# Performance work log

Measured on AMD Instinct MI355X. Metric: run time of the kernel, lower is better.

The kernel has to match this reference:

```python
import jax, jax.numpy as jnp
import numpy as np

B, C, H, W = 4, 512, 128, 128
CI = C // 2   # inter_planes
CQ = C // 8   # q/k dim in CrossAttention


def conv1x1(x, w, b=None):
    # x: [B,Cin,H,W], w: [Cout,Cin]
    y = jnp.einsum('oc,bchw->bohw', w, x)
    if b is not None:
        y = y + b[None, :, None, None]
    return y


def setup_inputs() -> dict:
    key = jax.random.key(0)
    ks = jax.random.split(key, 13)
    s = 0.05
    return {
        'x': jax.random.normal(ks[0], (B, C, H, W), jnp.float32),
        # SCCA gating params (1x1 convs, no bias except conv_up)
        'w_q_right': jax.random.normal(ks[1], (1, C), jnp.float32) * s,
        'w_v_right': jax.random.normal(ks[2], (CI, C), jnp.float32) * s,
        'w_up': jax.random.normal(ks[3], (C, CI), jnp.float32) * s,
        'b_up': jnp.zeros((C,), jnp.float32),
        'w_q_left': jax.random.normal(ks[4], (CI, C), jnp.float32) * s,
        'w_v_left': jax.random.normal(ks[5], (CI, C), jnp.float32) * s,
        # CrossAttention params (1x1 convs with bias)
        'wq': jax.random.normal(ks[6], (CQ, C), jnp.float32) * s,
        'bq': jnp.zeros((CQ,), jnp.float32),
        'wk': jax.random.normal(ks[7], (CQ, C), jnp.float32) * s,
        'bk': jnp.zeros((CQ,), jnp.float32),
        'wv': jax.random.normal(ks[8], (C, C), jnp.float32) * s,
        'bv': jnp.zeros((C,), jnp.float32),
        'gamma': jnp.asarray(0.5, jnp.float32),
    }


def cross_attention(x, wq, bq, wk, bk, wv, bv, gamma):
    # criss-cross attention: each pixel attends to its row and column
    b, c, h, w = x.shape
    q = conv1x1(x, wq, bq)   # [B,CQ,H,W]
    k = conv1x1(x, wk, bk)   # [B,CQ,H,W]
    v = conv1x1(x, wv, bv)   # [B,C,H,W]
    # column (H) affinities with -inf on the self diagonal (as in INF())
    diag = jnp.where(jnp.eye(h, dtype=bool), -jnp.inf, 0.0).astype(x.dtype)
    e_h = jnp.einsum('bchw,bcgw->bhwg', q, k) + diag[None, :, None, :]  # [B,H,W,H]
    e_w = jnp.einsum('bchw,bchv->bhwv', q, k)                            # [B,H,W,W]
    att = jax.nn.softmax(jnp.concatenate([e_h, e_w], axis=-1), axis=-1)  # [B,H,W,H+W]
    a_h, a_w = att[..., :h], att[..., h:]
    out_h = jnp.einsum('bcgw,bhwg->bchw', v, a_h)
    out_w = jnp.einsum('bchv,bhwv->bchw', v, a_w)
    return gamma * (out_h + out_w) + x


def spatial_weighted(x, w_q_right, w_v_right, w_up, b_up):
    b, c, h, w = x.shape
    input_x = conv1x1(x, w_v_right).reshape(b, CI, h * w)       # [B,CI,HW]
    mask = jax.nn.softmax(conv1x1(x, w_q_right).reshape(b, h * w), axis=-1)  # [B,HW]
    ctx = jnp.einsum('bcn,bn->bc', input_x, mask)               # [B,CI]
    ctx = jnp.einsum('oc,bc->bo', w_up, ctx) + b_up             # [B,C]
    mask_ch = jax.nn.sigmoid(ctx)[:, :, None, None]
    return x * mask_ch


def channel_weighted(x, w_q_left, w_v_left):
    b, c, h, w = x.shape
    g_x = conv1x1(x, w_q_left)                                  # [B,CI,H,W]
    avg = g_x.mean(axis=(2, 3))                                 # [B,CI]
    theta = conv1x1(x, w_v_left).reshape(b, CI, h * w)          # [B,CI,HW]
    ctx = jax.nn.softmax(jnp.einsum('bc,bcn->bn', avg, theta), axis=-1)
    mask_sp = jax.nn.sigmoid(ctx).reshape(b, 1, h, w)
    return x * mask_sp


def reference(x, w_q_right, w_v_right, w_up, b_up, w_q_left, w_v_left,
              wq, bq, wk, bk, wv, bv, gamma):
    cc = spatial_weighted(x, w_q_right, w_v_right, w_up, b_up)
    cc = cross_attention(cc, wq, bq, wk, bk, wv, bv, gamma)
    cs = channel_weighted(x, w_q_left, w_v_left)
    cs = cross_attention(cs, wq, bq, wk, bk, wv, bv, gamma)
    out = cs + cc
    out = cross_attention(out, wq, bq, wk, bk, wv, bv, gamma)
    return out
```

## Files before the change

kernel.cpp:

```cpp
#include <hip/hip_runtime.h>
#include <hip/hip_bf16.h>
#include <math.h>

typedef __hip_bfloat16 bf16;
typedef __attribute__((ext_vector_type(8))) short s16x8;
typedef __attribute__((ext_vector_type(4))) float f32x4;

constexpr int Bn  = 4;
constexpr int Cn  = 512;
constexpr int Hn  = 128;
constexpr int Wn  = 128;
constexpr int Nn  = Hn * Wn;
constexpr int CQn = 64;
constexpr int CIn = 256;

__device__ __forceinline__ float bf2f(bf16 v){ return __bfloat162float(v); }
__device__ __forceinline__ bf16  f2bf(float v){ return __float2bfloat16(v); }

__device__ __forceinline__ void gload_lds16(const void* g, void* l){
  __builtin_amdgcn_global_load_lds(
      (const __attribute__((address_space(1))) unsigned int*)g,
      (__attribute__((address_space(3))) unsigned int*)l,
      16, 0, 0);
}


__global__ __launch_bounds__(256) void k_dotc2(const float* __restrict__ x,
                                               const float* __restrict__ w,
                                               int wstride,
                                               float* __restrict__ part){
  int t = blockIdx.x * 256 + threadIdx.x;
  int half = blockIdx.y;
  int b = t >> 14;
  const float* wp = w + (size_t)b * wstride + half * 256;
  const float* xp = x + (size_t)b * Cn * Nn + (size_t)(half * 256) * Nn + (t & (Nn - 1));
  float acc = 0.f;
  #pragma unroll 16
  for (int c = 0; c < 256; ++c) acc += wp[c] * xp[(size_t)c * Nn];
  part[(size_t)half * (Bn * Nn) + t] = acc;
}

__global__ __launch_bounds__(256) void k_dotcadd(const float* __restrict__ part,
                                                 float* __restrict__ out){
  int t = blockIdx.x * 256 + threadIdx.x;
  out[t] = part[t] + part[(size_t)Bn * Nn + t];
}

__global__ __launch_bounds__(256) void k_rowmean(const float* __restrict__ x,
                                                 float* __restrict__ out,
                                                 float scale){
  int bc = blockIdx.x;
  const float* xp = x + (size_t)bc * Nn;
  float acc = 0.f;
  for (int n = threadIdx.x; n < Nn; n += 256) acc += xp[n];
  for (int o = 32; o > 0; o >>= 1) acc += __shfl_down(acc, o);
  __shared__ float red[4];
  if ((threadIdx.x & 63) == 0) red[threadIdx.x >> 6] = acc;
  __syncthreads();
  if (threadIdx.x == 0) out[bc] = (red[0] + red[1] + red[2] + red[3]) * scale;
}

__global__ __launch_bounds__(256) void k_rowdot(const float* __restrict__ W,
                                                const float* __restrict__ vec,
                                                float* __restrict__ out){
  __shared__ float vs[Cn];
  int b = blockIdx.x, t = threadIdx.x;
  for (int j = t; j < Cn; j += 256) vs[j] = vec[b * Cn + j];
  __syncthreads();
  const float4* wp = (const float4*)(W + (size_t)t * Cn);
  float a = 0.f;
  #pragma unroll 4
  for (int j = 0; j < Cn / 4; ++j){
    float4 w4 = wp[j];
    a += w4.x * vs[4*j] + w4.y * vs[4*j+1] + w4.z * vs[4*j+2] + w4.w * vs[4*j+3];
  }
  out[b * CIn + t] = a;
}

__global__ __launch_bounds__(256) void k_coldot(const float* __restrict__ W,
                                                const float* __restrict__ vec,
                                                float* __restrict__ out){
  __shared__ float vs[CIn];
  int b = blockIdx.y, t = threadIdx.x;
  int c = blockIdx.x * 256 + t;
  if (t < CIn) vs[t] = vec[b * CIn + t];
  __syncthreads();
  float a = 0.f;
  #pragma unroll 8
  for (int j = 0; j < CIn; ++j) a += W[(size_t)j * Cn + c] * vs[j];
  out[b * Cn + c] = a;
}

__global__ __launch_bounds__(256) void k_mch2(const float* __restrict__ w_up,
                                              const float* __restrict__ b_up,
                                              const float* __restrict__ ctx,
                                              float* __restrict__ mch){
  __shared__ float cs[CIn];
  int b = blockIdx.y, t = threadIdx.x;
  int o = blockIdx.x * 256 + t;
  if (t < CIn) cs[t] = ctx[b * CIn + t];
  __syncthreads();
  const float4* wp = (const float4*)(w_up + (size_t)o * CIn);
  float a = b_up[o];
  #pragma unroll 4
  for (int j = 0; j < CIn / 4; ++j){
    float4 w4 = wp[j];
    a += w4.x * cs[4*j] + w4.y * cs[4*j+1] + w4.z * cs[4*j+2] + w4.w * cs[4*j+3];
  }
  mch[b * Cn + o] = 1.f / (1.f + expf(-a));
}

__global__ __launch_bounds__(1024) void k_stats(const float* __restrict__ vv,
                                                float* __restrict__ stats){
  int b = blockIdx.x;
  const float* pp = vv + (size_t)b * Nn;
  int t = threadIdx.x;
  float m = -3.4e38f;
  for (int n = t; n < Nn; n += 1024) m = fmaxf(m, pp[n]);
  for (int o = 32; o > 0; o >>= 1) m = fmaxf(m, __shfl_down(m, o));
  __shared__ float red[16];
  int wid = t >> 6, lid = t & 63;
  if (lid == 0) red[wid] = m;
  __syncthreads();
  if (t == 0){
    float q = red[0];
    for (int i = 1; i < 16; i++) q = fmaxf(q, red[i]);
    red[0] = q;
  }
  __syncthreads();
  m = red[0];
  __syncthreads();
  float s = 0.f;
  for (int n = t; n < Nn; n += 1024) s += expf(pp[n] - m);
  for (int o = 32; o > 0; o >>= 1) s += __shfl_down(s, o);
  if (lid == 0) red[wid] = s;
  __syncthreads();
  if (t == 0){
    float q = 0.f;
    for (int i = 0; i < 16; i++) q += red[i];
    stats[b * 2]     = m;
    stats[b * 2 + 1] = q;
  }
}

__global__ __launch_bounds__(256) void k_weighted(const float* __restrict__ x,
                                                  const float* __restrict__ logits,
                                                  const float* __restrict__ stats,
                                                  float* __restrict__ out){
  int bc = blockIdx.x;
  int b = bc >> 9;
  const float* xp = x + (size_t)bc * Nn;
  const float* lp = logits + (size_t)b * Nn;
  float m = stats[b * 2], den = stats[b * 2 + 1];
  float acc = 0.f;
  for (int n = threadIdx.x; n < Nn; n += 256) acc += xp[n] * expf(lp[n] - m);
  for (int o = 32; o > 0; o >>= 1) acc += __shfl_down(acc, o);
  __shared__ float red[4];
  if ((threadIdx.x & 63) == 0) red[threadIdx.x >> 6] = acc;
  __syncthreads();
  if (threadIdx.x == 0) out[bc] = (red[0] + red[1] + red[2] + red[3]) / den;
}

__global__ __launch_bounds__(256) void k_msp(const float* __restrict__ lg,
                                             const float* __restrict__ stats,
                                             float* __restrict__ msp){
  int t = blockIdx.x * 256 + threadIdx.x;
  int b = t >> 14;
  float v = expf(lg[t] - stats[b * 2]) / stats[b * 2 + 1];
  msp[t] = 1.f / (1.f + expf(-v));
}


__global__ __launch_bounds__(256) void k_cvt_w(const float* __restrict__ in,
                                               bf16* __restrict__ out, int n){
  int t = blockIdx.x * 256 + threadIdx.x;
  if (t < n) out[t] = f2bf(in[t]);
}

__global__ __launch_bounds__(256) void k_prep_wqk(const float* __restrict__ wq,
                                                  const float* __restrict__ wk,
                                                  const float* __restrict__ bq,
                                                  const float* __restrict__ bk,
                                                  bf16* __restrict__ wqk_hi,
                                                  bf16* __restrict__ wqk_lo,
                                                  float* __restrict__ bqk){
  int t = blockIdx.x * 256 + threadIdx.x;
  int o = t >> 9, c = t & 511;
  float v = (o < 64) ? wq[(size_t)o * Cn + c] : wk[(size_t)(o - 64) * Cn + c];
  bf16 h = f2bf(v);
  wqk_hi[t] = h;
  wqk_lo[t] = f2bf(v - bf2f(h));
  if (t < 128) bqk[t] = (t < 64) ? bq[t] : bk[t - 64];
}

__global__ __launch_bounds__(256) void k_prep_wqk_mch(const float* __restrict__ wq,
                                                      const float* __restrict__ wk,
                                                      const float* __restrict__ mch,
                                                      bf16* __restrict__ hi,
                                                      bf16* __restrict__ lo){
  int t = blockIdx.x * 256 + threadIdx.x;
  int b = t >> 16;
  int oc = t & 65535;
  int o = oc >> 9, c = oc & 511;
  float w = (o < 64) ? wq[(size_t)o * Cn + c] : wk[(size_t)(o - 64) * Cn + c];
  float v = w * mch[b * Cn + c];
  bf16 h = f2bf(v);
  hi[t] = h;
  lo[t] = f2bf(v - bf2f(h));
}

__global__ __launch_bounds__(256) void k_prep_wv_mch(const float* __restrict__ wv,
                                                     const float* __restrict__ mch,
                                                     bf16* __restrict__ out){
  int t = blockIdx.x * 256 + threadIdx.x;
  int b = t >> 18;
  int oc = t & 262143;
  int c = oc & 511;
  out[t] = f2bf(wv[oc] * mch[b * Cn + c]);
}

__global__ __launch_bounds__(256) void k_cvt_T(const float* __restrict__ in,
                                               bf16* __restrict__ out_hi,
                                               bf16* __restrict__ out_lo){
  __shared__ bf16 th_[32][33];
  __shared__ bf16 tl_[32][33];
  int nt = blockIdx.x, ct = blockIdx.y, b = blockIdx.z;
  int n0 = nt * 32, c0 = ct * 32;
  int t = threadIdx.x;
  #pragma unroll
  for (int kk = 0; kk < 4; ++kk){
    int idx = t + kk * 256;
    int cl = idx >> 5, nl = idx & 31;
    float v = in[((size_t)(b * Cn + c0 + cl)) * Nn + n0 + nl];
    bf16 h = f2bf(v);
    th_[cl][nl] = h;
    tl_[cl][nl] = f2bf(v - bf2f(h));
  }
  __syncthreads();
  #pragma unroll
  for (int kk = 0; kk < 4; ++kk){
    int idx = t + kk * 256;
    int nl = idx >> 5, cl = idx & 31;
    size_t o = ((size_t)(b * Nn + n0 + nl)) * Cn + c0 + cl;
    out_hi[o] = th_[cl][nl];
    out_lo[o] = tl_[cl][nl];
  }
}


__global__ __launch_bounds__(256) void k_v_mfma(const bf16* __restrict__ xT,
                                                const bf16* __restrict__ wvb,
                                                int wstride,
                                                const float* __restrict__ bv,
                                                const float* __restrict__ nscale,
                                                bf16* __restrict__ v){
  __shared__ short As[128 * 64];
  __shared__ short Bs[128 * 64];
  __shared__ float bvs[128];
  int lin = blockIdx.x;
  int swz = (lin & 7) * 256 + (lin >> 3);
  int cb = (swz & 3) * 128;
  int nb = ((swz >> 2) & 127) * 128;
  int b  = swz >> 9;
  int t = threadIdx.x, lane = t & 63, wid = t >> 6;
  int wm = wid >> 1, wn = wid & 1;
  int l15 = lane & 15, l4 = lane >> 4;
  if (t < 128) bvs[t] = bv[cb + t];
  f32x4 acc[4][4];
  #pragma unroll
  for (int i = 0; i < 4; i++)
    #pragma unroll
    for (int j = 0; j < 4; j++) acc[i][j] = (f32x4){0.f, 0.f, 0.f, 0.f};

  const bf16* wp = wvb + (size_t)b * wstride + (size_t)cb * Cn;
  const bf16* xp = xT + ((size_t)b * Nn + nb) * Cn;
  int r8 = lane >> 3;
  int kc = (lane & 7) * 8;
  for (int kt = 0; kt < 8; ++kt){
    int k0 = kt * 64;
    #pragma unroll
    for (int j = 0; j < 4; ++j){
      int inst = wid * 4 + j;
      int row = inst * 8 + r8;
      gload_lds16(wp + (size_t)row * Cn + k0 + kc, (char*)As + inst * 1024);
      gload_lds16(xp + (size_t)row * Cn + k0 + kc, (char*)Bs + inst * 1024);
    }
    __syncthreads();
    #pragma unroll
    for (int kk = 0; kk < 64; kk += 32){
      s16x8 a[4], bb[4];
      #pragma unroll
      for (int mi = 0; mi < 4; mi++)
        a[mi] = *(const s16x8*)&As[(wm * 64 + mi * 16 + l15) * 64 + kk + l4 * 8];
      #pragma unroll
      for (int ni = 0; ni < 4; ni++)
        bb[ni] = *(const s16x8*)&Bs[(wn * 64 + ni * 16 + l15) * 64 + kk + l4 * 8];
      #pragma unroll
      for (int mi = 0; mi < 4; mi++)
        #pragma unroll
        for (int ni = 0; ni < 4; ni++)
          acc[mi][ni] = __builtin_amdgcn_mfma_f32_16x16x32_bf16(a[mi], bb[ni], acc[mi][ni], 0, 0, 0);
    }
    __syncthreads();
  }
  float sc[4];
  #pragma unroll
  for (int ni = 0; ni < 4; ni++)
    sc[ni] = nscale ? nscale[(size_t)b * Nn + nb + wn * 64 + ni * 16 + l15] : 1.f;
  #pragma unroll
  for (int mi = 0; mi < 4; mi++){
    #pragma unroll
    for (int r = 0; r < 4; r++){
      int cl = wm * 64 + mi * 16 + l4 * 4 + r;
      int c  = cb + cl;
      float bias = bvs[cl];
      #pragma unroll
      for (int ni = 0; ni < 4; ni++){
        int n = nb + wn * 64 + ni * 16 + l15;
        v[((size_t)(b * Cn + c)) * Nn + n] = f2bf(acc[mi][ni][r] * sc[ni] + bias);
      }
    }
  }
}

__global__ __launch_bounds__(256) void k_qk_mfma(const bf16* __restrict__ xT_hi,
                                                 const bf16* __restrict__ xT_lo,
                                                 const bf16* __restrict__ wqk_hi,
                                                 const bf16* __restrict__ wqk_lo,
                                                 int wstride,
                                                 const float* __restrict__ bqk,
                                                 const float* __restrict__ nscale,
                                                 bf16* __restrict__ qhw,
                                                 bf16* __restrict__ khw){
  __shared__ char smem[65536];
  short* Ah = (short*)smem;
  short* Al = Ah + 8192;
  short* Bh = Al + 8192;
  short* Bl = Bh + 8192;
  char*  Os = smem;
  __shared__ float bs[128];
  int h = blockIdx.x, b = blockIdx.y;
  int nb = h * 128;
  int t = threadIdx.x, lane = t & 63, wid = t >> 6;
  int wm = wid >> 1, wn = wid & 1;
  int l15 = lane & 15, l4 = lane >> 4;
  if (t < 128) bs[t] = bqk[t];
  f32x4 acc[4][4];
  #pragma unroll
  for (int i = 0; i < 4; i++)
    #pragma unroll
    for (int j = 0; j < 4; j++) acc[i][j] = (f32x4){0.f, 0.f, 0.f, 0.f};

  const bf16* wh = wqk_hi + (size_t)b * wstride;
  const bf16* wl = wqk_lo + (size_t)b * wstride;
  const bf16* xh = xT_hi + ((size_t)b * Nn + nb) * Cn;
  const bf16* xl = xT_lo + ((size_t)b * Nn + nb) * Cn;
  int r8 = lane >> 3;
  int kc = (lane & 7) * 8;
  for (int kt = 0; kt < 8; ++kt){
    int k0 = kt * 64;
    #pragma unroll
    for (int j = 0; j < 4; ++j){
      int inst = wid * 4 + j;
      int row = inst * 8 + r8;
      size_t off = (size_t)row * Cn + k0 + kc;
      gload_lds16(wh + off, (char*)Ah + inst * 1024);
      gload_lds16(wl + off, (char*)Al + inst * 1024);
      gload_lds16(xh + off, (char*)Bh + inst * 1024);
      gload_lds16(xl + off, (char*)Bl + inst * 1024);
    }
    __syncthreads();
    #pragma unroll
    for (int kk = 0; kk < 64; kk += 32){
      s16x8 ah[4], al[4], bh[4], bl[4];
      #pragma unroll
      for (int mi = 0; mi < 4; mi++){
        int idx = (wm * 64 + mi * 16 + l15) * 64 + kk + l4 * 8;
        ah[mi] = *(const s16x8*)&Ah[idx];
        al[mi] = *(const s16x8*)&Al[idx];
      }
      #pragma unroll
      for (int ni = 0; ni < 4; ni++){
        int idx = (wn * 64 + ni * 16 + l15) * 64 + kk + l4 * 8;
        bh[ni] = *(const s16x8*)&Bh[idx];
        bl[ni] = *(const s16x8*)&Bl[idx];
      }
      #pragma unroll
      for (int mi = 0; mi < 4; mi++)
        #pragma unroll
        for (int ni = 0; ni < 4; ni++){
          acc[mi][ni] = __builtin_amdgcn_mfma_f32_16x16x32_bf16(ah[mi], bh[ni], acc[mi][ni], 0, 0, 0);
          acc[mi][ni] = __builtin_amdgcn_mfma_f32_16x16x32_bf16(ah[mi], bl[ni], acc[mi][ni], 0, 0, 0);
          acc[mi][ni] = __builtin_amdgcn_mfma_f32_16x16x32_bf16(al[mi], bh[ni], acc[mi][ni], 0, 0, 0);
        }
    }
    __syncthreads();
  }
  float sc[4];
  #pragma unroll
  for (int ni = 0; ni < 4; ni++)
    sc[ni] = nscale ? nscale[(size_t)b * Nn + nb + wn * 64 + ni * 16 + l15] : 1.f;
  #pragma unroll
  for (int mi = 0; mi < 4; mi++){
    #pragma unroll
    for (int r = 0; r < 4; r++){
      int o = wm * 64 + mi * 16 + l4 * 4 + r;
      float bias = bs[o];
      #pragma unroll
      for (int ni = 0; ni < 4; ni++){
        int n = wn * 64 + ni * 16 + l15;
        bf16 bv = f2bf(acc[mi][ni][r] * sc[ni] + bias);
        int byte = (n * 256 + o * 2) ^ ((n & 7) << 4);
        *(unsigned short*)(Os + byte) = *(unsigned short*)&bv;
      }
    }
  }
  __syncthreads();
  #pragma unroll
  for (int i = 0; i < 8; ++i){
    int s = t + i * 256;
    int row = s >> 3, seg = s & 7;
    int w = row & 127, qk = row >> 7;
    int o0 = qk * 64 + seg * 8;
    int byte = (w * 256 + o0 * 2) ^ ((w & 7) << 4);
    s16x8 d = *(const s16x8*)(Os + byte);
    bf16* dst = (qk == 0 ? qhw : khw) + (((size_t)b * Wn + w) * Hn + h) * CQn + seg * 8;
    *(s16x8*)dst = d;
  }
}


__global__ __launch_bounds__(256) void k_att_h(const bf16* __restrict__ qhw,
                                               const bf16* __restrict__ khw,
                                               const bf16* __restrict__ vT,
                                               float* __restrict__ mh,
                                               float* __restrict__ sh,
                                               bf16* __restrict__ ohX){
  __shared__ char smem[65536];
  char* attb = smem;
  char* vbb  = smem + 32768;
  float* redm = (float*)(smem + 32768);
  float* reds = redm + 256;
  int w = blockIdx.x, b = blockIdx.y;
  int t = threadIdx.x, lane = t & 63, wid = t >> 6;
  int wm = wid >> 1, wn = wid & 1;
  int l15 = lane & 15, l4 = lane >> 4;

  const bf16* qp = qhw + ((size_t)(b * Wn + w)) * (Hn * CQn);
  const bf16* kp = khw + ((size_t)(b * Wn + w)) * (Hn * CQn);
  f32x4 acc[4][4];
  #pragma unroll
  for (int i = 0; i < 4; i++)
    #pragma unroll
    for (int j = 0; j < 4; j++) acc[i][j] = (f32x4){0.f, 0.f, 0.f, 0.f};
  #pragma unroll
  for (int kk = 0; kk < 64; kk += 32){
    s16x8 a[4], bb[4];
    #pragma unroll
    for (int mi = 0; mi < 4; mi++)
      a[mi] = *(const s16x8*)(qp + (size_t)(wm * 64 + mi * 16 + l15) * CQn + kk + l4 * 8);
    #pragma unroll
    for (int ni = 0; ni < 4; ni++)
      bb[ni] = *(const s16x8*)(kp + (size_t)(wn * 64 + ni * 16 + l15) * CQn + kk + l4 * 8);
    #pragma unroll
    for (int mi = 0; mi < 4; mi++)
      #pragma unroll
      for (int ni = 0; ni < 4; ni++)
        acc[mi][ni] = __builtin_amdgcn_mfma_f32_16x16x32_bf16(a[mi], bb[ni], acc[mi][ni], 0, 0, 0);
  }
  if (wm == wn){
    #pragma unroll
    for (int mi = 0; mi < 4; mi++)
      #pragma unroll
      for (int r = 0; r < 4; r++)
        if (l15 == l4 * 4 + r) acc[mi][mi][r] = -1e30f;
  }
  float rm[4][4];
  #pragma unroll
  for (int mi = 0; mi < 4; mi++)
    #pragma unroll
    for (int r = 0; r < 4; r++){
      float m = fmaxf(fmaxf(acc[mi][0][r], acc[mi][1][r]),
                      fmaxf(acc[mi][2][r], acc[mi][3][r]));
      m = fmaxf(m, __shfl_xor(m, 1));
      m = fmaxf(m, __shfl_xor(m, 2));
      m = fmaxf(m, __shfl_xor(m, 4));
      m = fmaxf(m, __shfl_xor(m, 8));
      rm[mi][r] = m;
    }
  if (l15 == 0){
    #pragma unroll
    for (int mi = 0; mi < 4; mi++)
      #pragma unroll
      for (int r = 0; r < 4; r++)
        redm[wn * 128 + wm * 64 + mi * 16 + l4 * 4 + r] = rm[mi][r];
  }
  __syncthreads();
  float rs[4][4];
  #pragma unroll
  for (int mi = 0; mi < 4; mi++)
    #pragma unroll
    for (int r = 0; r < 4; r++){
      int h = wm * 64 + mi * 16 + l4 * 4 + r;
      float m = fmaxf(redm[h], redm[128 + h]);
      rm[mi][r] = m;
      float s = 0.f;
      #pragma unroll
      for (int ni = 0; ni < 4; ni++){
        acc[mi][ni][r] = expf(acc[mi][ni][r] - m);
        s += acc[mi][ni][r];
      }
      s += __shfl_xor(s, 1);
      s += __shfl_xor(s, 2);
      s += __shfl_xor(s, 4);
      s += __shfl_xor(s, 8);
      rs[mi][r] = s;
    }
  if (l15 == 0){
    #pragma unroll
    for (int mi = 0; mi < 4; mi++)
      #pragma unroll
      for (int r = 0; r < 4; r++)
        reds[wn * 128 + wm * 64 + mi * 16 + l4 * 4 + r] = rs[mi][r];
  }
  __syncthreads();
  #pragma unroll
  for (int mi = 0; mi < 4; mi++)
    #pragma unroll
    for (int r = 0; r < 4; r++){
      int h = wm * 64 + mi * 16 + l4 * 4 + r;
      if (wn == 0 && l15 == 0){
        mh[(size_t)(b * Wn + w) * Hn + h] = rm[mi][r];
        sh[(size_t)(b * Wn + w) * Hn + h] = reds[h] + reds[128 + h];
      }
      #pragma unroll
      for (int ni = 0; ni < 4; ni++){
        int g = wn * 64 + ni * 16 + l15;
        bf16 bv = f2bf(acc[mi][ni][r]);
        int byte = (h * 256 + g * 2) ^ ((h & 7) << 4);
        *(unsigned short*)(attb + byte) = *(unsigned short*)&bv;
      }
    }
  __syncthreads();
  for (int cb = 0; cb < Cn; cb += 128){
    const bf16* vp = vT + ((size_t)(b * Wn + w) * Cn + cb) * Hn;
    for (int s = t; s < 2048; s += 256){
      int row = s >> 4, seg = s & 15;
      s16x8 d = *(const s16x8*)(vp + (size_t)row * Hn + seg * 8);
      int byte = (row * 256 + seg * 16) ^ ((row & 7) << 4);
      *(s16x8*)(vbb + byte) = d;
    }
    __syncthreads();
    f32x4 acc2[4][4];
    #pragma unroll
    for (int i = 0; i < 4; i++)
      #pragma unroll
      for (int j = 0; j < 4; j++) acc2[i][j] = (f32x4){0.f, 0.f, 0.f, 0.f};
    #pragma unroll
    for (int kk = 0; kk < 128; kk += 32){
      s16x8 a[4], bb[4];
      #pragma unroll
      for (int mi = 0; mi < 4; mi++){
        int row = wm * 64 + mi * 16 + l15;
        int byte = (row * 256 + (kk + l4 * 8) * 2) ^ ((row & 7) << 4);
        a[mi] = *(const s16x8*)(vbb + byte);
      }
      #pragma unroll
      for (int ni = 0; ni < 4; ni++){
        int row = wn * 64 + ni * 16 + l15;
        int byte = (row * 256 + (kk + l4 * 8) * 2) ^ ((row & 7) << 4);
        bb[ni] = *(const s16x8*)(attb + byte);
      }
      #pragma unroll
      for (int mi = 0; mi < 4; mi++)
        #pragma unroll
        for (int ni = 0; ni < 4; ni++)
          acc2[mi][ni] = __builtin_amdgcn_mfma_f32_16x16x32_bf16(a[mi], bb[ni], acc2[mi][ni], 0, 0, 0);
    }
    bf16* op = ohX + ((size_t)(b * Cn + cb)) * Nn + (size_t)w * Hn;
    #pragma unroll
    for (int mi = 0; mi < 4; mi++)
      #pragma unroll
      for (int r = 0; r < 4; r++){
        int cl = wm * 64 + mi * 16 + l4 * 4 + r;
        #pragma unroll
        for (int ni = 0; ni < 4; ni++){
          int h = wn * 64 + ni * 16 + l15;
          op[(size_t)cl * Nn + h] = f2bf(acc2[mi][ni][r]);
        }
      }
    __syncthreads();
  }
}

__global__ __launch_bounds__(256) void k_att_w(const bf16* __restrict__ qhw,
                                               const bf16* __restrict__ khw,
                                               const bf16* __restrict__ v,
                                               float* __restrict__ mw,
                                               float* __restrict__ sw,
                                               bf16* __restrict__ ow){
  __shared__ char smem[65536];
  char* attb = smem;
  char* vbb  = smem + 32768;
  float* redm = (float*)(smem + 32768);
  float* reds = redm + 256;
  int h = blockIdx.x, b = blockIdx.y;
  int t = threadIdx.x, lane = t & 63, wid = t >> 6;
  int wm = wid >> 1, wn = wid & 1;
  int l15 = lane & 15, l4 = lane >> 4;

  const bf16* qp = qhw + (size_t)b * Wn * Hn * CQn + (size_t)h * CQn;
  const bf16* kp = khw + (size_t)b * Wn * Hn * CQn + (size_t)h * CQn;
  f32x4 acc[4][4];
  #pragma unroll
  for (int i = 0; i < 4; i++)
    #pragma unroll
    for (int j = 0; j < 4; j++) acc[i][j] = (f32x4){0.f, 0.f, 0.f, 0.f};
  #pragma unroll
  for (int kk = 0; kk < 64; kk += 32){
    s16x8 a[4], bb[4];
    #pragma unroll
    for (int mi = 0; mi < 4; mi++)
      a[mi] = *(const s16x8*)(qp + (size_t)(wm * 64 + mi * 16 + l15) * (Hn * CQn) + kk + l4 * 8);
    #pragma unroll
    for (int ni = 0; ni < 4; ni++)
      bb[ni] = *(const s16x8*)(kp + (size_t)(wn * 64 + ni * 16 + l15) * (Hn * CQn) + kk + l4 * 8);
    #pragma unroll
    for (int mi = 0; mi < 4; mi++)
      #pragma unroll
      for (int ni = 0; ni < 4; ni++)
        acc[mi][ni] = __builtin_amdgcn_mfma_f32_16x16x32_bf16(a[mi], bb[ni], acc[mi][ni], 0, 0, 0);
  }
  float rm[4][4];
  #pragma unroll
  for (int mi = 0; mi < 4; mi++)
    #pragma unroll
    for (int r = 0; r < 4; r++){
      float m = fmaxf(fmaxf(acc[mi][0][r], acc[mi][1][r]),
                      fmaxf(acc[mi][2][r], acc[mi][3][r]));
      m = fmaxf(m, __shfl_xor(m, 1));
      m = fmaxf(m, __shfl_xor(m, 2));
      m = fmaxf(m, __shfl_xor(m, 4));
      m = fmaxf(m, __shfl_xor(m, 8));
      rm[mi][r] = m;
    }
  if (l15 == 0){
    #pragma unroll
    for (int mi = 0; mi < 4; mi++)
      #pragma unroll
      for (int r = 0; r < 4; r++)
        redm[wn * 128 + wm * 64 + mi * 16 + l4 * 4 + r] = rm[mi][r];
  }
  __syncthreads();
  float rs[4][4];
  #pragma unroll
  for (int mi = 0; mi < 4; mi++)
    #pragma unroll
    for (int r = 0; r < 4; r++){
      int wr = wm * 64 + mi * 16 + l4 * 4 + r;
      float m = fmaxf(redm[wr], redm[128 + wr]);
      rm[mi][r] = m;
      float s = 0.f;
      #pragma unroll
      for (int ni = 0; ni < 4; ni++){
        acc[mi][ni][r] = expf(acc[mi][ni][r] - m);
        s += acc[mi][ni][r];
      }
      s += __shfl_xor(s, 1);
      s += __shfl_xor(s, 2);
      s += __shfl_xor(s, 4);
      s += __shfl_xor(s, 8);
      rs[mi][r] = s;
    }
  if (l15 == 0){
    #pragma unroll
    for (int mi = 0; mi < 4; mi++)
      #pragma unroll
      for (int r = 0; r < 4; r++)
        reds[wn * 128 + wm * 64 + mi * 16 + l4 * 4 + r] = rs[mi][r];
  }
  __syncthreads();
  #pragma unroll
  for (int mi = 0; mi < 4; mi++)
    #pragma unroll
    for (int r = 0; r < 4; r++){
      int wr = wm * 64 + mi * 16 + l4 * 4 + r;
      if (wn == 0 && l15 == 0){
        mw[(size_t)(b * Hn + h) * Wn + wr] = rm[mi][r];
        sw[(size_t)(b * Hn + h) * Wn + wr] = reds[wr] + reds[128 + wr];
      }
      #pragma unroll
      for (int ni = 0; ni < 4; ni++){
        int g = wn * 64 + ni * 16 + l15;
        bf16 bv = f2bf(acc[mi][ni][r]);
        int byte = (wr * 256 + g * 2) ^ ((wr & 7) << 4);
        *(unsigned short*)(attb + byte) = *(unsigned short*)&bv;
      }
    }
  __syncthreads();
  for (int cb = 0; cb < Cn; cb += 128){
    const bf16* vp = v + (size_t)(b * Cn + cb) * Nn + (size_t)h * Wn;
    for (int s = t; s < 2048; s += 256){
      int row = s >> 4, seg = s & 15;
      s16x8 d = *(const s16x8*)(vp + (size_t)row * Nn + seg * 8);
      int byte = (row * 256 + seg * 16) ^ ((row & 7) << 4);
      *(s16x8*)(vbb + byte) = d;
    }
    __syncthreads();
    f32x4 acc2[4][4];
    #pragma unroll
    for (int i = 0; i < 4; i++)
      #pragma unroll
      for (int j = 0; j < 4; j++) acc2[i][j] = (f32x4){0.f, 0.f, 0.f, 0.f};
    #pragma unroll
    for (int kk = 0; kk < 128; kk += 32){
      s16x8 a[4], bb[4];
      #pragma unroll
      for (int mi = 0; mi < 4; mi++){
        int row = wm * 64 + mi * 16 + l15;
        int byte = (row * 256 + (kk + l4 * 8) * 2) ^ ((row & 7) << 4);
        a[mi] = *(const s16x8*)(vbb + byte);
      }
      #pragma unroll
      for (int ni = 0; ni < 4; ni++){
        int row = wn * 64 + ni * 16 + l15;
        int byte = (row * 256 + (kk + l4 * 8) * 2) ^ ((row & 7) << 4);
        bb[ni] = *(const s16x8*)(attb + byte);
      }
      #pragma unroll
      for (int mi = 0; mi < 4; mi++)
        #pragma unroll
        for (int ni = 0; ni < 4; ni++)
          acc2[mi][ni] = __builtin_amdgcn_mfma_f32_16x16x32_bf16(a[mi], bb[ni], acc2[mi][ni], 0, 0, 0);
    }
    bf16* op = ow + (size_t)(b * Cn + cb) * Nn + (size_t)h * Wn;
    #pragma unroll
    for (int mi = 0; mi < 4; mi++)
      #pragma unroll
      for (int r = 0; r < 4; r++){
        int cl = wm * 64 + mi * 16 + l4 * 4 + r;
        #pragma unroll
        for (int ni = 0; ni < 4; ni++){
          int wr = wn * 64 + ni * 16 + l15;
          op[(size_t)cl * Nn + wr] = f2bf(acc2[mi][ni][r]);
        }
      }
    __syncthreads();
  }
}

__global__ __launch_bounds__(256) void k_alpha(const float* __restrict__ mh,
                                               const float* __restrict__ sh,
                                               const float* __restrict__ mw,
                                               const float* __restrict__ sw,
                                               float* __restrict__ ahT,
                                               float* __restrict__ aw){
  int t = blockIdx.x * 256 + threadIdx.x;
  int b = t >> 14;
  int hw = t & (Nn - 1);
  int h = hw >> 7, w = hw & 127;
  size_t ih = (size_t)(b * Wn + w) * Hn + h;
  size_t iw = t;
  float mhv = mh[ih], mwv = mw[iw];
  float M = fmaxf(mhv, mwv);
  float eh_ = expf(mhv - M), ew_ = expf(mwv - M);
  float inv = 1.f / (sh[ih] * eh_ + sw[iw] * ew_);
  ahT[t] = eh_ * inv;
  aw[t]  = ew_ * inv;
}


__global__ __launch_bounds__(256) void k_trans(const bf16* __restrict__ in,
                                               bf16* __restrict__ out,
                                               int CH){
  __shared__ unsigned short tile[64][72];
  int tl = blockIdx.x, c = blockIdx.y, b = blockIdx.z;
  int th = tl >> 1, tw = tl & 1;
  int h0 = th * 64, w0 = tw * 64;
  int t = threadIdx.x;
  const bf16* ip = in + ((size_t)(b * CH + c)) * Nn;
  {
    int hl = t >> 2, wq = (t & 3) * 16;
    const bf16* src = ip + (size_t)(h0 + hl) * Wn + w0 + wq;
    s16x8 d0 = *(const s16x8*)(src);
    s16x8 d1 = *(const s16x8*)(src + 8);
    #pragma unroll
    for (int j = 0; j < 8; ++j){
      tile[wq + j][hl]     = (unsigned short)d0[j];
      tile[wq + 8 + j][hl] = (unsigned short)d1[j];
    }
  }
  __syncthreads();
  {
    int wl = t >> 2, hq = (t & 3) * 16;
    s16x8 d0 = *(const s16x8*)&tile[wl][hq];
    s16x8 d1 = *(const s16x8*)&tile[wl][hq + 8];
    bf16* dst = out + ((size_t)(b * Wn + w0 + wl) * CH + c) * Hn + h0 + hq;
    *(s16x8*)(dst)     = d0;
    *(s16x8*)(dst + 8) = d1;
  }
}

__global__ __launch_bounds__(256) void k_fuse2(const float* __restrict__ in,
                                               const bf16* __restrict__ ohX,
                                               const bf16* __restrict__ ow,
                                               const float* __restrict__ ahT,
                                               const float* __restrict__ aw,
                                               const float* __restrict__ gamma,
                                               float* __restrict__ out){
  __shared__ unsigned short tileT[64][138];
  int c = blockIdx.x, half = blockIdx.y, b = blockIdx.z;
  int t = threadIdx.x;
  float g = gamma[0];
  int h0 = half * 64;
  const bf16* ohp = ohX + ((size_t)(b * Cn + c)) * Nn;
  #pragma unroll
  for (int i = 0; i < 4; ++i){
    int s = t + i * 256;
    int w = s >> 3, seg = s & 7;
    s16x8 d = *(const s16x8*)(ohp + (size_t)w * Hn + h0 + seg * 8);
    #pragma unroll
    for (int j = 0; j < 8; ++j)
      tileT[seg * 8 + j][w] = (unsigned short)d[j];
  }
  __syncthreads();
  size_t base = ((size_t)(b * Cn + c)) * Nn;
  #pragma unroll
  for (int i = 0; i < 8; ++i){
    int o = t + i * 256;
    int hl = o >> 5, w4 = (o & 31) * 4;
    int h = h0 + hl;
    size_t idx = base + (size_t)h * Wn + w4;
    size_t aidx = (size_t)b * Nn + (size_t)h * Wn + w4;
    ushort4 owv = *(const ushort4*)((const unsigned short*)ow + idx);
    float4 ah4 = *(const float4*)(ahT + aidx);
    float4 aw4 = *(const float4*)(aw + aidx);
    float4 inv = in ? *(const float4*)(in + idx) : (float4){0.f,0.f,0.f,0.f};
    float r[4];
    #pragma unroll
    for (int j = 0; j < 4; ++j){
      unsigned short uh = tileT[hl][w4 + j];
      unsigned short uo = ((const unsigned short*)&owv)[j];
      float ohv = bf2f(*(bf16*)&uh);
      float owf = bf2f(*(bf16*)&uo);
      float ahv = ((const float*)&ah4)[j];
      float awv = ((const float*)&aw4)[j];
      r[j] = g * (ahv * ohv + awv * owf) + ((const float*)&inv)[j];
    }
    float4 o4 = { r[0], r[1], r[2], r[3] };
    *(float4*)(out + idx) = o4;
  }
}

__global__ __launch_bounds__(512) void k_fuse3(const float* __restrict__ x,
                                               const float* __restrict__ mch,
                                               const float* __restrict__ msp,
                                               const bf16* __restrict__ oh1,
                                               const bf16* __restrict__ ow1,
                                               const float* __restrict__ a1h,
                                               const float* __restrict__ a1w,
                                               const bf16* __restrict__ oh2,
                                               const bf16* __restrict__ ow2,
                                               const float* __restrict__ a2h,
                                               const float* __restrict__ a2w,
                                               const float* __restrict__ gamma,
                                               float* __restrict__ out){
  __shared__ unsigned short tl_[64][138];
  int c = blockIdx.x, half = blockIdx.y, b = blockIdx.z;
  int t = threadIdx.x;
  float g = gamma[0];
  float mc = mch[b * Cn + c];
  int h0 = half * 64;
  const bf16* p1 = oh1 + ((size_t)(b * Cn + c)) * Nn;
  const bf16* p2 = oh2 + ((size_t)(b * Cn + c)) * Nn;
  size_t base = ((size_t)(b * Cn + c)) * Nn;
  #pragma unroll
  for (int i = 0; i < 2; ++i){
    int s = t + i * 512;
    int w = s >> 3, seg = s & 7;
    s16x8 d = *(const s16x8*)(p2 + (size_t)w * Hn + h0 + seg * 8);
    #pragma unroll
    for (int j = 0; j < 8; ++j)
      tl_[seg * 8 + j][w] = (unsigned short)d[j];
  }
  __syncthreads();
  float r[4][4];
  #pragma unroll
  for (int i = 0; i < 4; ++i){
    int o = t + i * 512;
    int hl = o >> 5, w4 = (o & 31) * 4;
    int h = h0 + hl;
    size_t idx = base + (size_t)h * Wn + w4;
    size_t aidx = (size_t)b * Nn + (size_t)h * Wn + w4;
    ushort4 o2v = *(const ushort4*)((const unsigned short*)ow2 + idx);
    float4 a2h4 = *(const float4*)(a2h + aidx);
    float4 a2w4 = *(const float4*)(a2w + aidx);
    float4 xv4  = *(const float4*)(x + idx);
    float4 mn4  = *(const float4*)(msp + aidx);
    #pragma unroll
    for (int j = 0; j < 4; ++j){
      unsigned short u2 = tl_[hl][w4 + j];
      unsigned short w2 = ((const unsigned short*)&o2v)[j];
      float oh2v = bf2f(*(bf16*)&u2), ow2v = bf2f(*(bf16*)&w2);
      float term2 = g * (((const float*)&a2h4)[j] * oh2v + ((const float*)&a2w4)[j] * ow2v);
      float resid = ((const float*)&xv4)[j] * (mc + ((const float*)&mn4)[j]);
      r[i][j] = term2 + resid;
    }
  }
  __syncthreads();
  #pragma unroll
  for (int i = 0; i < 2; ++i){
    int s = t + i * 512;
    int w = s >> 3, seg = s & 7;
    s16x8 d = *(const s16x8*)(p1 + (size_t)w * Hn + h0 + seg * 8);
    #pragma unroll
    for (int j = 0; j < 8; ++j)
      tl_[seg * 8 + j][w] = (unsigned short)d[j];
  }
  __syncthreads();
  #pragma unroll
  for (int i = 0; i < 4; ++i){
    int o = t + i * 512;
    int hl = o >> 5, w4 = (o & 31) * 4;
    int h = h0 + hl;
    size_t idx = base + (size_t)h * Wn + w4;
    size_t aidx = (size_t)b * Nn + (size_t)h * Wn + w4;
    ushort4 o1v = *(const ushort4*)((const unsigned short*)ow1 + idx);
    float4 a1h4 = *(const float4*)(a1h + aidx);
    float4 a1w4 = *(const float4*)(a1w + aidx);
    float rr[4];
    #pragma unroll
    for (int j = 0; j < 4; ++j){
      unsigned short u1 = tl_[hl][w4 + j];
      unsigned short w1 = ((const unsigned short*)&o1v)[j];
      float oh1v = bf2f(*(bf16*)&u1), ow1v = bf2f(*(bf16*)&w1);
      float term1 = g * (((const float*)&a1h4)[j] * oh1v + ((const float*)&a1w4)[j] * ow1v);
      rr[j] = r[i][j] + term1;
    }
    float4 o4 = { rr[0], rr[1], rr[2], rr[3] };
    *(float4*)(out + idx) = o4;
  }
}


static void run_att(const bf16* xT_hi, const bf16* xT_lo,
                    const bf16* wqk_hi, const bf16* wqk_lo, int wqk_bstride,
                    const float* bqk,
                    const bf16* wvb, int wv_bstride, const float* bv,
                    const float* nscale,
                    bf16* qhw, bf16* khw, bf16* v, bf16* vT,
                    float* mh, float* sh, float* mw, float* sw,
                    float* ahT, float* aw, bf16* tmp, hipStream_t stream){
  bf16* ohX = tmp;
  bf16* ow  = tmp + (size_t)Bn * Cn * Nn;
  k_qk_mfma<<<dim3(Nn / 128, Bn), 256, 0, stream>>>(xT_hi, xT_lo, wqk_hi, wqk_lo,
                                                    wqk_bstride, bqk, nscale,
                                                    qhw, khw);
  k_v_mfma<<<2048, 256, 0, stream>>>(xT_hi, wvb, wv_bstride, bv, nscale, v);
  k_trans<<<dim3(4, Cn, Bn), 256, 0, stream>>>(v, vT, Cn);
  k_att_h<<<dim3(Wn, Bn), 256, 0, stream>>>(qhw, khw, vT, mh, sh, ohX);
  k_att_w<<<dim3(Hn, Bn), 256, 0, stream>>>(qhw, khw, v, mw, sw, ow);
  k_alpha<<<Bn * Nn / 256, 256, 0, stream>>>(mh, sh, mw, sw, ahT, aw);
}

extern "C" void kernel_launch(void* const* d_in, const int* in_sizes, int n_in,
                              void* d_out, int out_size, void* d_ws, size_t ws_size,
                              hipStream_t stream){
  (void)in_sizes; (void)n_in; (void)out_size; (void)ws_size;
  const float* x         = (const float*)d_in[0];
  const float* w_q_right = (const float*)d_in[1];
  const float* w_v_right = (const float*)d_in[2];
  const float* w_up      = (const float*)d_in[3];
  const float* b_up      = (const float*)d_in[4];
  const float* w_q_left  = (const float*)d_in[5];
  const float* w_v_left  = (const float*)d_in[6];
  const float* wq        = (const float*)d_in[7];
  const float* bq        = (const float*)d_in[8];
  const float* wk        = (const float*)d_in[9];
  const float* bk        = (const float*)d_in[10];
  const float* wv        = (const float*)d_in[11];
  const float* bv        = (const float*)d_in[12];
  const float* gamma     = (const float*)d_in[13];

  const size_t SZ_MAP = (size_t)Bn * Cn * Nn;
  char* p = (char*)d_ws;
  float* buf0   = (float*)p; p += SZ_MAP * 4;
  float* buf1   = (float*)p; p += SZ_MAP * 4;
  bf16*  vbuf   = (bf16*)p;  p += SZ_MAP * 2;
  bf16*  vT     = (bf16*)p;  p += SZ_MAP * 2;
  bf16*  qhw    = (bf16*)p;  p += (size_t)Bn * CQn * Nn * 2;
  bf16*  khw    = (bf16*)p;  p += (size_t)Bn * CQn * Nn * 2;
  float* ebuf   = (float*)p; p += (size_t)SZ_MAP * 2;
  float* logits = (float*)p; p += (size_t)Bn * Nn * 4;
  float* ctxlog = (float*)p; p += (size_t)Bn * Nn * 4;
  float* msp    = (float*)p; p += (size_t)Bn * Nn * 4;
  float* xbar   = (float*)p; p += Bn * Cn * 4;
  float* wgt    = (float*)p; p += Bn * Cn * 4;
  float* u      = (float*)p; p += Bn * Cn * 4;
  float* mch    = (float*)p; p += Bn * Cn * 4;
  float* avg    = (float*)p; p += Bn * CIn * 4;
  float* ctx    = (float*)p; p += Bn * CIn * 4;
  float* stats_sp = (float*)p; p += 64;
  float* stats_ch = (float*)p; p += 64;
  bf16*  wvb    = (bf16*)p;  p += (size_t)Cn * Cn * 2;
  bf16*  wqk_hi = (bf16*)p;  p += (size_t)128 * Cn * 2;
  bf16*  wqk_lo = (bf16*)p;  p += (size_t)128 * Cn * 2;
  float* bqk    = (float*)p; p += 128 * 4;
  float* mh     = (float*)p; p += (size_t)Bn * Nn * 4;
  float* sh     = (float*)p; p += (size_t)Bn * Nn * 4;
  float* mw     = (float*)p; p += (size_t)Bn * Nn * 4;
  float* sw     = (float*)p; p += (size_t)Bn * Nn * 4;
  float* ah1    = (float*)p; p += (size_t)Bn * Nn * 4;
  float* aw1    = (float*)p; p += (size_t)Bn * Nn * 4;
  float* ah2    = (float*)p; p += (size_t)Bn * Nn * 4;
  float* aw2    = (float*)p; p += (size_t)Bn * Nn * 4;
  float* dpart  = (float*)p; p += (size_t)2 * Bn * Nn * 4;
  bf16*  wqk_mch_hi = (bf16*)p; p += (size_t)Bn * 128 * Cn * 2;
  bf16*  wqk_mch_lo = (bf16*)p; p += (size_t)Bn * 128 * Cn * 2;
  bf16*  wv_mch     = (bf16*)p; p += (size_t)Bn * Cn * Cn * 2;

  bf16*  xT_hi  = (bf16*)ebuf;
  bf16*  xT_lo  = (bf16*)buf1;
  bf16*  xT_hi3 = (bf16*)ebuf;
  bf16*  xT_lo3 = (bf16*)d_out;

  k_cvt_w<<<(Cn * Cn + 255) / 256, 256, 0, stream>>>(wv, wvb, Cn * Cn);
  k_prep_wqk<<<(128 * Cn) / 256, 256, 0, stream>>>(wq, wk, bq, bk, wqk_hi, wqk_lo, bqk);
  k_cvt_T<<<dim3(Nn / 32, Cn / 32, Bn), 256, 0, stream>>>(x, xT_hi, xT_lo);

  k_dotc2<<<dim3(Bn * Nn / 256, 2), 256, 0, stream>>>(x, w_q_right, 0, dpart);
  k_dotcadd<<<Bn * Nn / 256, 256, 0, stream>>>(dpart, logits);
  k_rowmean<<<Bn * Cn, 256, 0, stream>>>(x, xbar, 1.f / Nn);
  k_rowdot<<<Bn, 256, 0, stream>>>(w_q_left, xbar, avg);
  k_coldot<<<dim3(Cn / 256, Bn), 256, 0, stream>>>(w_v_left, avg, u);
  k_stats<<<Bn, 1024, 0, stream>>>(logits, stats_sp);
  k_weighted<<<Bn * Cn, 256, 0, stream>>>(x, logits, stats_sp, wgt);
  k_rowdot<<<Bn, 256, 0, stream>>>(w_v_right, wgt, ctx);
  k_mch2<<<dim3(Cn / 256, Bn), 256, 0, stream>>>(w_up, b_up, ctx, mch);
  k_prep_wqk_mch<<<(Bn * 128 * Cn) / 256, 256, 0, stream>>>(wq, wk, mch,
                                                            wqk_mch_hi, wqk_mch_lo);
  k_prep_wv_mch<<<(Bn * Cn * Cn) / 256, 256, 0, stream>>>(wv, mch, wv_mch);
  k_dotc2<<<dim3(Bn * Nn / 256, 2), 256, 0, stream>>>(x, u, Cn, dpart);
  k_dotcadd<<<Bn * Nn / 256, 256, 0, stream>>>(dpart, ctxlog);
  k_stats<<<Bn, 1024, 0, stream>>>(ctxlog, stats_ch);
  k_msp<<<Bn * Nn / 256, 256, 0, stream>>>(ctxlog, stats_ch, msp);

  run_att(xT_hi, xT_lo, wqk_mch_hi, wqk_mch_lo, 128 * Cn, bqk,
          wv_mch, Cn * Cn, bv, nullptr,
          qhw, khw, vbuf, vT, mh, sh, mw, sw, ah1, aw1, (bf16*)d_out, stream);
  run_att(xT_hi, xT_lo, wqk_hi, wqk_lo, 0, bqk, wvb, 0, bv, msp,
          qhw, khw, vbuf, vT, mh, sh, mw, sw, ah2, aw2, (bf16*)buf0, stream);
  k_fuse3<<<dim3(Cn, 2, Bn), 512, 0, stream>>>(x, mch, msp,
                                               (const bf16*)d_out,
                                               (const bf16*)d_out + SZ_MAP, ah1, aw1,
                                               (const bf16*)buf0,
                                               (const bf16*)buf0 + SZ_MAP, ah2, aw2,
                                               gamma, buf1);
  k_cvt_T<<<dim3(Nn / 32, Cn / 32, Bn), 256, 0, stream>>>(buf1, xT_hi3, xT_lo3);
  run_att(xT_hi3, xT_lo3, wqk_hi, wqk_lo, 0, bqk, wvb, 0, bv, nullptr,
          qhw, khw, vbuf, vT, mh, sh, mw, sw, ah1, aw1, (bf16*)buf0, stream);
  k_fuse2<<<dim3(Cn, 2, Bn), 256, 0, stream>>>(buf1, (const bf16*)buf0,
                                               (const bf16*)buf0 + SZ_MAP, ah1, aw1,
                                               gamma, (float*)d_out);
}
```

Before: 1.214 ms.

## Fuse the two first-stage branch projections into shared-input dual-GEMM kernels

The first two criss-cross attention passes use the same transposed input. Their Q/K projections and their V projections are now computed together: one kernel loads each input tile once and accumulates against both weight sets, where before there were two separate run_att projection passes. The attention, transpose and alpha kernels are then launched explicitly for each branch, with new aliased scratch buffers for the second branch. This removes a second full read of the transposed activations and some launch overhead. In exchange it doubles accumulator register pressure, which may lower occupancy, and it adds delicate buffer aliasing within buf0 and buf1.

Result: slower. 1.296 ms (+6.7%).

```diff
diff --git a/kernel.cpp b/kernel.cpp
--- a/kernel.cpp
+++ b/kernel.cpp
@@ -318,6 +318,99 @@
       for (int ni = 0; ni < 4; ni++){
         int n = nb + wn * 64 + ni * 16 + l15;
         v[((size_t)(b * Cn + c)) * Nn + n] = f2bf(acc[mi][ni][r] * sc[ni] + bias);
+      }
+    }
+  }
+}
+
+__global__ __launch_bounds__(256) void k_v_mfma2(const bf16* __restrict__ xT,
+                                                 const bf16* __restrict__ w1,
+                                                 const bf16* __restrict__ w2,
+                                                 const float* __restrict__ bv,
+                                                 const float* __restrict__ nscale2,
+                                                 bf16* __restrict__ v1,
+                                                 bf16* __restrict__ v2){
+  __shared__ short As1[128 * 64];
+  __shared__ short As2[128 * 64];
+  __shared__ short Bs[128 * 64];
+  __shared__ float bvs[128];
+  int lin = blockIdx.x;
+  int swz = (lin & 7) * 256 + (lin >> 3);
+  int cb = (swz & 3) * 128;
+  int nb = ((swz >> 2) & 127) * 128;
+  int b  = swz >> 9;
+  int t = threadIdx.x, lane = t & 63, wid = t >> 6;
+  int wm = wid >> 1, wn = wid & 1;
+  int l15 = lane & 15, l4 = lane >> 4;
+  if (t < 128) bvs[t] = bv[cb + t];
+  f32x4 acc1[4][4], acc2[4][4];
+  #pragma unroll
+  for (int i = 0; i < 4; i++)
+    #pragma unroll
+    for (int j = 0; j < 4; j++){
+      acc1[i][j] = (f32x4){0.f, 0.f, 0.f, 0.f};
+      acc2[i][j] = (f32x4){0.f, 0.f, 0.f, 0.f};
+    }
+
+  const bf16* p1 = w1 + (size_t)b * (Cn * Cn) + (size_t)cb * Cn;
+  const bf16* p2 = w2 + (size_t)cb * Cn;
+  const bf16* xp = xT + ((size_t)b * Nn + nb) * Cn;
+  int r8 = lane >> 3;
+  int kc = (lane & 7) * 8;
+  for (int kt = 0; kt < 8; ++kt){
+    int k0 = kt * 64;
+    #pragma unroll
+    for (int j = 0; j < 4; ++j){
+      int inst = wid * 4 + j;
+      int row = inst * 8 + r8;
+      size_t off = (size_t)row * Cn + k0 + kc;
+      gload_lds16(p1 + off, (char*)As1 + inst * 1024);
+      gload_lds16(p2 + off, (char*)As2 + inst * 1024);
+      gload_lds16(xp + off, (char*)Bs  + inst * 1024);
+    }
+    __syncthreads();
+    #pragma unroll
+    for (int kk = 0; kk < 64; kk += 32){
+      s16x8 bb[4], a1[4], a2[4];
+      #pragma unroll
+      for (int ni = 0; ni < 4; ni++)
+        bb[ni] = *(const s16x8*)&Bs[(wn * 64 + ni * 16 + l15) * 64 + kk + l4 * 8];
+      #pragma unroll
+      for (int mi = 0; mi < 4; mi++){
+        int idx = (wm * 64 + mi * 16 + l15) * 64 + kk + l4 * 8;
+        a1[mi] = *(const s16x8*)&As1[idx];
+        a2[mi] = *(const s16x8*)&As2[idx];
+      }
+      #pragma unroll
+      for (int mi = 0; mi < 4; mi++)
+        #pragma unroll
+        for (int ni = 0; ni < 4; ni++)
+          acc1[mi][ni] = __builtin_amdgcn_mfma_f32_16x16x32_bf16(a1[mi], bb[ni], acc1[mi][ni], 0, 0, 0);
+      #pragma unroll
+      for (int mi = 0; mi < 4; mi++)
+        #pragma unroll
+        for (int ni = 0; ni < 4; ni++)
+          acc2[mi][ni] = __builtin_amdgcn_mfma_f32_16x16x32_bf16(a2[mi], bb[ni], acc2[mi][ni], 0, 0, 0);
+    }
+    __syncthreads();
+  }
+  float sc[4];
+  #pragma unroll
+  for (int ni = 0; ni < 4; ni++)
+    sc[ni] = nscale2[(size_t)b * Nn + nb + wn * 64 + ni * 16 + l15];
+  #pragma unroll
+  for (int mi = 0; mi < 4; mi++){
+    #pragma unroll
+    for (int r = 0; r < 4; r++){
+      int cl = wm * 64 + mi * 16 + l4 * 4 + r;
+      int c  = cb + cl;
+      float bias = bvs[cl];
+      #pragma unroll
+      for (int ni = 0; ni < 4; ni++){
+        int n = nb + wn * 64 + ni * 16 + l15;
+        size_t o = ((size_t)(b * Cn + c)) * Nn + n;
+        v1[o] = f2bf(acc1[mi][ni][r] + bias);
+        v2[o] = f2bf(acc2[mi][ni][r] * sc[ni] + bias);
       }
     }
   }
@@ -425,6 +518,157 @@
     int byte = (w * 256 + o0 * 2) ^ ((w & 7) << 4);
     s16x8 d = *(const s16x8*)(Os + byte);
     bf16* dst = (qk == 0 ? qhw : khw) + (((size_t)b * Wn + w) * Hn + h) * CQn + seg * 8;
+    *(s16x8*)dst = d;
+  }
+}
+
+__global__ __launch_bounds__(256) void k_qk_mfma2(const bf16* __restrict__ xT_hi,
+                                                  const bf16* __restrict__ xT_lo,
+                                                  const bf16* __restrict__ w1_hi,
+                                                  const bf16* __restrict__ w1_lo,
+                                                  const bf16* __restrict__ w2_hi,
+                                                  const bf16* __restrict__ w2_lo,
+                                                  const float* __restrict__ bqk,
+                                                  const float* __restrict__ nscale2,
+                                                  bf16* __restrict__ q1,
+                                                  bf16* __restrict__ k1,
+                                                  bf16* __restrict__ q2,
+                                                  bf16* __restrict__ k2){
+  __shared__ char smem[49152];
+  short* A1h = (short*)smem;
+  char*  Os  = smem;
+  __shared__ float bs[128];
+  int h = blockIdx.x, b = blockIdx.y;
+  int nb = h * 128;
+  int t = threadIdx.x, lane = t & 63, wid = t >> 6;
+  int wm = wid >> 1, wn = wid & 1;
+  int l15 = lane & 15, l4 = lane >> 4;
+  if (t < 128) bs[t] = bqk[t];
+  f32x4 acc1[4][4], acc2[4][4];
+  #pragma unroll
+  for (int i = 0; i < 4; i++)
+    #pragma unroll
+    for (int j = 0; j < 4; j++){
+      acc1[i][j] = (f32x4){0.f, 0.f, 0.f, 0.f};
+      acc2[i][j] = (f32x4){0.f, 0.f, 0.f, 0.f};
+    }
+  const bf16* s0 = w1_hi + (size_t)b * (128 * Cn);
+  const bf16* s1 = w1_lo + (size_t)b * (128 * Cn);
+  const bf16* s2 = w2_hi;
+  const bf16* s3 = w2_lo;
+  const bf16* s4 = xT_hi + ((size_t)b * Nn + nb) * Cn;
+  const bf16* s5 = xT_lo + ((size_t)b * Nn + nb) * Cn;
+  int r4 = lane >> 2;
+  int kc = (lane & 3) * 8;
+  for (int kt = 0; kt < 16; ++kt){
+    int k0 = kt * 32;
+    #pragma unroll
+    for (int j = 0; j < 12; ++j){
+      int g = wid * 12 + j;
+      int tile = g >> 3, sub = g & 7;
+      const bf16* sp = (tile == 0) ? s0 : (tile == 1) ? s1 : (tile == 2) ? s2
+                     : (tile == 3) ? s3 : (tile == 4) ? s4 : s5;
+      int row = sub * 16 + r4;
+      gload_lds16(sp + (size_t)row * Cn + k0 + kc,
+                  (char*)A1h + tile * 8192 + sub * 1024);
+    }
+    __syncthreads();
+    {
+      s16x8 bh[4], bl[4], ah[4], al[4];
+      #pragma unroll
+      for (int ni = 0; ni < 4; ni++){
+        int idx = (wn * 64 + ni * 16 + l15) * 32 + l4 * 8;
+        bh[ni] = *(const s16x8*)&A1h[4 * 4096 + idx];
+        bl[ni] = *(const s16x8*)&A1h[5 * 4096 + idx];
+      }
+      #pragma unroll
+      for (int mi = 0; mi < 4; mi++){
+        int idx = (wm * 64 + mi * 16 + l15) * 32 + l4 * 8;
+        ah[mi] = *(const s16x8*)&A1h[idx];
+        al[mi] = *(const s16x8*)&A1h[4096 + idx];
+      }
+      #pragma unroll
+      for (int mi = 0; mi < 4; mi++)
+        #pragma unroll
+        for (int ni = 0; ni < 4; ni++){
+          acc1[mi][ni] = __builtin_amdgcn_mfma_f32_16x16x32_bf16(ah[mi], bh[ni], acc1[mi][ni], 0, 0, 0);
+          acc1[mi][ni] = __builtin_amdgcn_mfma_f32_16x16x32_bf16(ah[mi], bl[ni], acc1[mi][ni], 0, 0, 0);
+          acc1[mi][ni] = __builtin_amdgcn_mfma_f32_16x16x32_bf16(al[mi], bh[ni], acc1[mi][ni], 0, 0, 0);
+        }
+      #pragma unroll
+      for (int mi = 0; mi < 4; mi++){
+        int idx = (wm * 64 + mi * 16 + l15) * 32 + l4 * 8;
+        ah[mi] = *(const s16x8*)&A1h[2 * 4096 + idx];
+        al[mi] = *(const s16x8*)&A1h[3 * 4096 + idx];
+      }
+      #pragma unroll
+      for (int mi = 0; mi < 4; mi++)
+        #pragma unroll
+        for (int ni = 0; ni < 4; ni++){
+          acc2[mi][ni] = __builtin_amdgcn_mfma_f32_16x16x32_bf16(ah[mi], bh[ni], acc2[mi][ni], 0, 0, 0);
+          acc2[mi][ni] = __builtin_amdgcn_mfma_f32_16x16x32_bf16(ah[mi], bl[ni], acc2[mi][ni], 0, 0, 0);
+          acc2[mi][ni] = __builtin_amdgcn_mfma_f32_16x16x32_bf16(al[mi], bh[ni], acc2[mi][ni], 0, 0, 0);
+        }
+    }
+    __syncthreads();
+  }
+  float sc[4];
+  #pragma unroll
+  for (int ni = 0; ni < 4; ni++)
+    sc[ni] = nscale2[(size_t)b * Nn + nb + wn * 64 + ni * 16 + l15];
+  #pragma unroll
+  for (int mi = 0; mi < 4; mi++){
+    #pragma unroll
+    for (int r = 0; r < 4; r++){
+      int o = wm * 64 + mi * 16 + l4 * 4 + r;
+      float bias = bs[o];
+      #pragma unroll
+      for (int ni = 0; ni < 4; ni++){
+        int n = wn * 64 + ni * 16 + l15;
+        bf16 bv = f2bf(acc1[mi][ni][r] + bias);
+        int byte = (n * 256 + o * 2) ^ ((n & 7) << 4);
+        *(unsigned short*)(Os + byte) = *(unsigned short*)&bv;
+      }
+    }
+  }
+  __syncthreads();
+  #pragma unroll
+  for (int i = 0; i < 8; ++i){
+    int s = t + i * 256;
+    int row = s >> 3, seg = s & 7;
+    int w = row & 127, qk = row >> 7;
+    int o0 = qk * 64 + seg * 8;
+    int byte = (w * 256 + o0 * 2) ^ ((w & 7) << 4);
+    s16x8 d = *(const s16x8*)(Os + byte);
+    bf16* dst = (qk == 0 ? q1 : k1) + (((size_t)b * Wn + w) * Hn + h) * CQn + seg * 8;
+    *(s16x8*)dst = d;
+  }
+  __syncthreads();
+  #pragma unroll
+  for (int mi = 0; mi < 4; mi++){
+    #pragma unroll
+    for (int r = 0; r < 4; r++){
+      int o = wm * 64 + mi * 16 + l4 * 4 + r;
+      float bias = bs[o];
+      #pragma unroll
+      for (int ni = 0; ni < 4; ni++){
+        int n = wn * 64 + ni * 16 + l15;
+        bf16 bv = f2bf(acc2[mi][ni][r] * sc[ni] + bias);
+        int byte = (n * 256 + o * 2) ^ ((n & 7) << 4);
+        *(unsigned short*)(Os + byte) = *(unsigned short*)&bv;
+      }
+    }
+  }
+  __syncthreads();
+  #pragma unroll
+  for (int i = 0; i < 8; ++i){
+    int s = t + i * 256;
+    int row = s >> 3, seg = s & 7;
+    int w = row & 127, qk = row >> 7;
+    int o0 = qk * 64 + seg * 8;
+    int byte = (w * 256 + o0 * 2) ^ ((w & 7) << 4);
+    s16x8 d = *(const s16x8*)(Os + byte);
+    bf16* dst = (qk == 0 ? q2 : k2) + (((size_t)b * Wn + w) * Hn + h) * CQn + seg * 8;
     *(s16x8*)dst = d;
   }
 }
@@ -1021,6 +1265,10 @@
 
   bf16*  xT_hi  = (bf16*)ebuf;
   bf16*  xT_lo  = (bf16*)buf1;
+  bf16*  vbuf2  = (bf16*)buf1;
+  bf16*  qhw2   = (bf16*)buf1 + SZ_MAP;
+  bf16*  khw2   = (bf16*)buf1 + SZ_MAP + (size_t)Bn * CQn * Nn;
+  bf16*  vT2    = (bf16*)buf0 + SZ_MAP;
   bf16*  xT_hi3 = (bf16*)ebuf;
   bf16*  xT_lo3 = (bf16*)d_out;
 
@@ -1045,16 +1293,26 @@
   k_stats<<<Bn, 1024, 0, stream>>>(ctxlog, stats_ch);
   k_msp<<<Bn * Nn / 256, 256, 0, stream>>>(ctxlog, stats_ch, msp);
 
-  run_att(xT_hi, xT_lo, wqk_mch_hi, wqk_mch_lo, 128 * Cn, bqk,
-          wv_mch, Cn * Cn, bv, nullptr,
-          qhw, khw, vbuf, vT, mh, sh, mw, sw, ah1, aw1, (bf16*)d_out, stream);
-  run_att(xT_hi, xT_lo, wqk_hi, wqk_lo, 0, bqk, wvb, 0, bv, msp,
-          qhw, khw, vbuf, vT, mh, sh, mw, sw, ah2, aw2, (bf16*)buf0, stream);
+  bf16* oh1 = (bf16*)d_out;
+  bf16* ow1 = (bf16*)d_out + SZ_MAP;
+  bf16* oh2 = (bf16*)buf0;
+  bf16* ow2 = (bf16*)buf0 + SZ_MAP;
+  k_qk_mfma2<<<dim3(Nn / 128, Bn), 256, 0, stream>>>(xT_hi, xT_lo,
+                                                     wqk_mch_hi, wqk_mch_lo,
+                                                     wqk_hi, wqk_lo, bqk, msp,
+                                                     qhw, khw, qhw2, khw2);
+  k_v_mfma2<<<2048, 256, 0, stream>>>(xT_hi, wv_mch, wvb, bv, msp, vbuf, vbuf2);
+  k_trans<<<dim3(4, Cn, Bn), 256, 0, stream>>>(vbuf, vT, Cn);
+  k_trans<<<dim3(4, Cn, Bn), 256, 0, stream>>>(vbuf2, vT2, Cn);
+  k_att_h<<<dim3(Wn, Bn), 256, 0, stream>>>(qhw, khw, vT, mh, sh, oh1);
+  k_att_w<<<dim3(Hn, Bn), 256, 0, stream>>>(qhw, khw, vbuf, mw, sw, ow1);
+  k_alpha<<<Bn * Nn / 256, 256, 0, stream>>>(mh, sh, mw, sw, ah1, aw1);
+  k_att_h<<<dim3(Wn, Bn), 256, 0, stream>>>(qhw2, khw2, vT2, mh, sh, oh2);
+  k_att_w<<<dim3(Hn, Bn), 256, 0, stream>>>(qhw2, khw2, vbuf2, mw, sw, ow2);
+  k_alpha<<<Bn * Nn / 256, 256, 0, stream>>>(mh, sh, mw, sw, ah2, aw2);
   k_fuse3<<<dim3(Cn, 2, Bn), 512, 0, stream>>>(x, mch, msp,
-                                               (const bf16*)d_out,
-                                               (const bf16*)d_out + SZ_MAP, ah1, aw1,
-                                               (const bf16*)buf0,
-                                               (const bf16*)buf0 + SZ_MAP, ah2, aw2,
+                                               oh1, ow1, ah1, aw1,
+                                               oh2, ow2, ah2, aw2,
                                                gamma, buf1);
   k_cvt_T<<<dim3(Nn / 32, Cn / 32, Bn), 256, 0, stream>>>(buf1, xT_hi3, xT_lo3);
   run_att(xT_hi3, xT_lo3, wqk_hi, wqk_lo, 0, bqk, wvb, 0, bv, nullptr,
```
